# Kernel tuning notes

Measured on AMD Instinct MI355X. Metric: run time of the kernel, lower is better.

Reference implementation:

```python
import jax, jax.numpy as jnp
import numpy as np

B, C, H, W = 2, 128, 64, 64
EPS = 1e-5


def setup_inputs() -> dict:
    key = jax.random.key(0)
    ks = jax.random.split(key, 8)
    sc = 1.0 / np.sqrt(C)
    inp = {
        "x": jax.random.normal(ks[0], (B, C, H, W, 2), jnp.float32),
        # naive complex BN affine params: per-channel, per-component (real/imag)
        "bn_w": jnp.ones((C, 2), jnp.float32),
        "bn_b": jnp.zeros((C, 2), jnp.float32),
        # complex 1x1 conv weights: (out_c, in_c, 2) -> [..,0]=W_real, [..,1]=W_imag
        "wq": jax.random.normal(ks[1], (C, C, 2), jnp.float32) * sc,
        "bq": jnp.zeros((C, 2), jnp.float32),
        "wk": jax.random.normal(ks[2], (C, C, 2), jnp.float32) * sc,
        "bk": jnp.zeros((C, 2), jnp.float32),
        "wv": jax.random.normal(ks[3], (C, C, 2), jnp.float32) * sc,
        "bv": jnp.zeros((C, 2), jnp.float32),
        "gamma": jnp.float32(0.05),
    }
    return inp


def _complex_bn(x, w, b):
    # naive complex BN: normalize real and imag independently per channel
    # x: (B,C,H,W,2); stats over (B,H,W) per (C, component)
    mean = x.mean(axis=(0, 2, 3), keepdims=True)
    var = x.var(axis=(0, 2, 3), keepdims=True)
    xn = (x - mean) * jax.lax.rsqrt(var + EPS)
    return xn * w[None, :, None, None, :] + b[None, :, None, None, :]


def _complex_conv1x1(x, w, b):
    # x: (B,C,H,W,2); w: (O,C,2); b: (O,2)
    xr, xi = x[..., 0], x[..., 1]
    wr, wi = w[..., 0], w[..., 1]
    yr = jnp.einsum('oc,bchw->bohw', wr, xr) - jnp.einsum('oc,bchw->bohw', wi, xi)
    yi = jnp.einsum('oc,bchw->bohw', wr, xi) + jnp.einsum('oc,bchw->bohw', wi, xr)
    yr = yr + b[:, 0][None, :, None, None]
    yi = yi + b[:, 1][None, :, None, None]
    return jnp.stack([yr, yi], axis=-1)


def _attention(x, wq, bq, wk, bk, wv, bv, gamma):
    scale = C ** (-0.5)
    N = H * W
    # q,k,v: (B,C,H,W,2) -> (B,C,N,2) -> (B,N,C,2)
    to_tokens = lambda t: t.reshape(B, C, N, 2).transpose(0, 2, 1, 3)
    q = to_tokens(_complex_conv1x1(x, wq, bq))
    k = to_tokens(_complex_conv1x1(x, wk, bk))
    v = to_tokens(_complex_conv1x1(x, wv, bv))

    qr, qi = q[..., 0], q[..., 1]          # (B,N,C)
    kr, ki = k[..., 0], -k[..., 1]         # conjugate of k
    # k_t = conj(k) with token/channel axes swapped -> (B,C,N)
    ktr = kr.transpose(0, 2, 1)
    kti = ki.transpose(0, 2, 1)

    # complex matmul q @ k_t -> only the real part is used downstream
    attn_real = jnp.einsum('bnc,bcm->bnm', qr, ktr) - jnp.einsum('bnc,bcm->bnm', qi, kti)
    attn_w = jax.nn.softmax(attn_real * scale, axis=-1)  # (B,N,N)
    # dropout = identity (eval mode)

    # attn is purely real -> complex matmul reduces to two real matmuls
    out_r = jnp.einsum('bnm,bmc->bnc', attn_w, v[..., 0])
    out_i = jnp.einsum('bnm,bmc->bnc', attn_w, v[..., 1])
    out = jnp.stack([out_r, out_i], axis=-1)              # (B,N,C,2)
    out = out.transpose(0, 2, 1, 3).reshape(B, C, H, W, 2)
    return x + gamma * out


def reference(x, bn_w, bn_b, wq, bq, wk, bk, wv, bv, gamma):
    xn = _complex_bn(x, bn_w, bn_b)
    return _attention(xn, wq, bq, wk, bk, wv, bv, gamma)
```

## Files before the change

### kernel.cpp

```cpp
#include <hip/hip_runtime.h>
#include <hip/hip_bf16.h>
#include <hip/hip_fp8.h>

typedef __bf16 bf16_t;
typedef __bf16 bf16x8 __attribute__((ext_vector_type(8)));
typedef float  f32x4  __attribute__((ext_vector_type(4)));
typedef long   i64_t;

#define MFMA16(A,B,C) __builtin_amdgcn_mfma_f32_16x16x32_bf16((A),(B),(C),0,0,0)
#define MFMA8(A,B,C)  __builtin_amdgcn_mfma_f32_16x16x32_fp8_fp8((A),(B),(C),0,0,0)
#define MFMA85(A,B,C) __builtin_amdgcn_mfma_f32_16x16x32_bf8_fp8((A),(B),(C),0,0,0)

constexpr int Bn = 2, Cc = 128, Hh = 64, Wd = 64;
constexpr int N  = Hh * Wd;
constexpr int T  = Bn * N;
constexpr int D  = 2 * Cc;
constexpr int NSP = 4;
constexpr float EPS = 1e-5f;
constexpr float SCL = 0.08838834764831845f * 1.4426950408889634f;
constexpr float PSH = 9.0f;

__device__ __forceinline__ int tfrag(int row, int ch) {
    return (((ch >> 5) * 4 + (row >> 4)) << 10) +
           ((((ch >> 3) & 3) * 16 + (row & 15)) << 4) + (ch & 7) * 2;
}

__device__ __forceinline__ void gl16(const void* g, void* l) {
    __builtin_amdgcn_global_load_lds(
        (const __attribute__((address_space(1))) void*)g,
        (__attribute__((address_space(3))) void*)l, 16, 0, 0);
}

__global__ void k_pre(const float* __restrict__ x, float4* __restrict__ part,
                      const float* __restrict__ wq, const float* __restrict__ wk,
                      const float* __restrict__ wv, const float* __restrict__ bq,
                      const float* __restrict__ bk, const float* __restrict__ bv,
                      char* __restrict__ Wg, float* __restrict__ bt) {
    int tid = threadIdx.x;
    if (blockIdx.x < 512) {
        int bid = blockIdx.x;
        int q = bid >> 7, c = bid & 127;
        float sr = 0.f, si = 0.f, qr = 0.f, qi = 0.f;
        for (int b = 0; b < Bn; ++b) {
            const float4* p = (const float4*)((const float2*)x +
                              (size_t)(b * Cc + c) * N + q * 1024);
            for (int i = tid; i < 512; i += 256) {
                float4 v = p[i];
                sr += v.x + v.z; si += v.y + v.w;
                qr += v.x * v.x + v.z * v.z; qi += v.y * v.y + v.w * v.w;
            }
        }
        #pragma unroll
        for (int d = 32; d >= 1; d >>= 1) {
            sr += __shfl_xor(sr, d); si += __shfl_xor(si, d);
            qr += __shfl_xor(qr, d); qi += __shfl_xor(qi, d);
        }
        __shared__ float red[4][4];
        int w = tid >> 6;
        if ((tid & 63) == 0) { red[w][0] = sr; red[w][1] = si; red[w][2] = qr; red[w][3] = qi; }
        __syncthreads();
        if (tid == 0) {
            part[c * 4 + q] = make_float4(red[0][0] + red[1][0] + red[2][0] + red[3][0],
                                          red[0][1] + red[1][1] + red[2][1] + red[3][1],
                                          red[0][2] + red[1][2] + red[2][2] + red[3][2],
                                          red[0][3] + red[1][3] + red[2][3] + red[3][3]);
        }
    } else {
        int o = blockIdx.x - 512;
        int k = tid;
        int proj = o >> 8, oc = o & 255;
        const float* wsrc = proj == 0 ? wq : (proj == 1 ? wk : wv);
        const float* bsrc = proj == 0 ? bq : (proj == 1 ? bk : bv);
        int co = oc >> 7, oo = oc & 127;
        int c = k & 127, kc = k >> 7;
        float val;
        if (co == 0) val = (kc == 0) ? wsrc[(oo * 128 + c) * 2 + 0] : -wsrc[(oo * 128 + c) * 2 + 1];
        else         val = (kc == 0) ? wsrc[(oo * 128 + c) * 2 + 1] :  wsrc[(oo * 128 + c) * 2 + 0];
        int tile = o >> 6, row = o & 63;
        *(bf16_t*)(Wg + (size_t)tile * 32768 + tfrag(row, k)) = (bf16_t)val;
        if (k == 0) bt[o] = bsrc[oo * 2 + co];
    }
}

__global__ void k_norm(const float* __restrict__ x, const float4* __restrict__ part,
                       const float* __restrict__ bn_w, const float* __restrict__ bn_b,
                       char* __restrict__ XNg) {
    __shared__ float4 ssl[128];
    __shared__ __align__(16) char Tsh[32768];
    int blk = blockIdx.x;
    int b = blk >> 6, hw0 = (blk & 63) * 64;
    int tid = threadIdx.x;
    if (tid < 128) {
        float4 p0 = part[tid * 4 + 0], p1 = part[tid * 4 + 1];
        float4 p2 = part[tid * 4 + 2], p3 = part[tid * 4 + 3];
        float sr = p0.x + p1.x + p2.x + p3.x, si = p0.y + p1.y + p2.y + p3.y;
        float qr = p0.z + p1.z + p2.z + p3.z, qi = p0.w + p1.w + p2.w + p3.w;
        const float inv = 1.0f / (float)(Bn * N);
        float mr = sr * inv, mi = si * inv;
        float vr = qr * inv - mr * mr, vi = qi * inv - mi * mi;
        float scr = bn_w[tid * 2 + 0] * rsqrtf(vr + EPS);
        float sci = bn_w[tid * 2 + 1] * rsqrtf(vi + EPS);
        ssl[tid] = make_float4(scr, bn_b[tid * 2 + 0] - mr * scr,
                               sci, bn_b[tid * 2 + 1] - mi * sci);
    }
    __syncthreads();
    const float4* xin4 = (const float4*)x;
    #pragma unroll
    for (int it = 0; it < 16; ++it) {
        int idx = it * 256 + tid;
        int c = idx >> 5, h2 = (idx & 31) * 2;
        size_t gi = ((size_t)(b * Cc + c) * N + hw0 + h2) >> 1;
        float4 v = xin4[gi];
        float4 s = ssl[c];
        *(bf16_t*)(Tsh + tfrag(h2, c))           = (bf16_t)(v.x * s.x + s.y);
        *(bf16_t*)(Tsh + tfrag(h2, c + 128))     = (bf16_t)(v.y * s.z + s.w);
        *(bf16_t*)(Tsh + tfrag(h2 + 1, c))       = (bf16_t)(v.z * s.x + s.y);
        *(bf16_t*)(Tsh + tfrag(h2 + 1, c + 128)) = (bf16_t)(v.w * s.z + s.w);
    }
    __syncthreads();
    #pragma unroll
    for (int it = 0; it < 8; ++it) {
        int idx = it * 256 + tid;
        *(uint4*)(XNg + (size_t)blk * 32768 + idx * 16) = *(const uint4*)(Tsh + idx * 16);
    }
}

__global__ __launch_bounds__(256) void k_qkv(const char* __restrict__ XNg,
        const char* __restrict__ Wg, const float* __restrict__ bt,
        char* __restrict__ Qg, char* __restrict__ Kg, char* __restrict__ Vg) {
    __shared__ __align__(16) char Xsh[32768];
    __shared__ __align__(16) char Wsh[32768];
    int mx = blockIdx.x, ny = blockIdx.y;
    int tid = threadIdx.x;
    int w = tid >> 6, lane = tid & 63, n15 = lane & 15, quad = lane >> 4;
    const char* xs = XNg + (size_t)mx * 32768;
    const char* wsp = Wg + (size_t)ny * 32768;
    #pragma unroll
    for (int i = 0; i < 8; ++i) {
        int off = (w * 8 + i) * 1024 + lane * 16;
        gl16(xs + off, Xsh + off);
        gl16(wsp + off, Wsh + off);
    }
    __syncthreads();
    f32x4 acc[4] = {};
    #pragma unroll
    for (int ks = 0; ks < 8; ++ks) {
        bf16x8 a = *(const bf16x8*)(Xsh + (ks * 4 + w) * 1024 + lane * 16);
        #pragma unroll
        for (int t = 0; t < 4; ++t) {
            bf16x8 bw = *(const bf16x8*)(Wsh + (ks * 4 + t) * 1024 + lane * 16);
            acc[t] = MFMA16(a, bw, acc[t]);
        }
    }
    int proj = ny >> 2;
    int jb = (ny & 3) * 64;
    __syncthreads();
    char* Osh = Xsh;
    #pragma unroll
    for (int t = 0; t < 4; ++t) {
        float bias = bt[ny * 64 + t * 16 + n15];
        unsigned w01 = (unsigned)__builtin_amdgcn_cvt_pk_fp8_f32(
            acc[t][0] + bias, acc[t][1] + bias, 0, false);
        unsigned w23 = (unsigned)__builtin_amdgcn_cvt_pk_fp8_f32(
            acc[t][2] + bias, acc[t][3] + bias, 0, false);
        unsigned char vb[4] = {(unsigned char)(w01 & 0xff), (unsigned char)((w01 >> 8) & 0xff),
                               (unsigned char)(w23 & 0xff), (unsigned char)((w23 >> 8) & 0xff)};
        #pragma unroll
        for (int r = 0; r < 4; ++r) {
            if (proj < 2) {
                int lf  = (t >> 1) * 4 + w;
                int lif = (((2 * t + (n15 >> 3)) & 3) << 4) + quad * 4 + r;
                Osh[lf * 512 + lif * 8 + (n15 & 7)] = vb[r];
            } else {
                int key = w * 16 + quad * 4 + r;
                int lf  = (w >> 1) * 4 + t;
                int lif = (((key >> 3) & 3) << 4) + n15;
                Osh[lf * 512 + lif * 8 + (key & 7)] = vb[r];
            }
        }
    }
    __syncthreads();
    {
        int lf = tid >> 5, sub = (tid & 31) * 16;
        size_t tile = (size_t)mx;
        int gfrag = (proj < 2) ? ((jb >> 5) * 4 + lf)
                               : ((lf >> 2) * 16 + (jb >> 4) + (lf & 3));
        char* dst = (proj == 0 ? Qg : (proj == 1 ? Kg : Vg));
        *(uint4*)(dst + tile * 16384 + (size_t)gfrag * 512 + sub) =
            *(const uint4*)(Osh + tid * 16);
    }
}

__global__ __launch_bounds__(256) void k_attn(const char* __restrict__ Qg,
        const char* __restrict__ Kg, const char* __restrict__ Vg,
        bf16_t* __restrict__ Opb, float* __restrict__ Lp) {
    __shared__ __align__(16) char Ksh[2 * 16384];
    __shared__ __align__(16) char Vsh[2 * 16384];
    __shared__ __align__(16) char Psh[4096];
    int bid = blockIdx.x;
    int grp = bid & 7, qt = bid >> 3;
    int sp = grp & 3, b = grp >> 2;
    int tid = threadIdx.x;
    int w = tid >> 6, lane = tid & 63, n15 = lane & 15, quad = lane >> 4;
    int r = w >> 1, h = w & 1;

    const i64_t ONES = 0x3838383838383838L;

    i64_t qf[2][8];
    const char* qb = Qg + (size_t)(b * 64 + qt) * 16384;
    #pragma unroll
    for (int g = 0; g < 2; ++g)
        #pragma unroll
        for (int ks = 0; ks < 8; ++ks)
            qf[g][ks] = *(const i64_t*)(qb + ((ks * 4 + r * 2 + g) << 9) + lane * 8);

    f32x4 o[2][8] = {};
    f32x4 l_[2] = {};

    size_t kbase = (size_t)(b * 64 + sp * 16) * 16384;
    #pragma unroll
    for (int i = 0; i < 4; ++i) {
        int off = (w * 4 + i) * 1024 + lane * 16;
        gl16(Kg + kbase + off, Ksh + off);
        gl16(Vg + kbase + off, Vsh + off);
    }

    for (int kt = 0; kt < 16; ++kt) {
        int cur = kt & 1;
        asm volatile("s_waitcnt vmcnt(0)" ::: "memory");
        __builtin_amdgcn_s_barrier();
        __builtin_amdgcn_sched_barrier(0);

        if (kt < 15) {
            size_t tb = kbase + (size_t)(kt + 1) * 16384;
            char* kb = Ksh + (cur ^ 1) * 16384;
            char* vb = Vsh + (cur ^ 1) * 16384;
            #pragma unroll
            for (int i = 0; i < 4; ++i) {
                int off = (w * 4 + i) * 1024 + lane * 16;
                gl16(Kg + tb + off, kb + off);
                gl16(Vg + tb + off, vb + off);
            }
        }

        const char* kc = Ksh + cur * 16384;
        f32x4 s[2][2] = {};
        #pragma unroll
        for (int ks = 0; ks < 8; ++ks) {
            #pragma unroll
            for (int c = 0; c < 2; ++c) {
                i64_t kf = *(const i64_t*)(kc + ((ks * 4 + h * 2 + c) << 9) + lane * 8);
                s[0][c] = MFMA8(qf[0][ks], kf, s[0][c]);
                s[1][c] = MFMA8(qf[1][ks], kf, s[1][c]);
            }
        }
        #pragma unroll
        for (int g = 0; g < 2; ++g)
            #pragma unroll
            for (int c = 0; c < 2; ++c) {
                float p0 = __builtin_amdgcn_exp2f(s[g][c][0] * SCL - PSH);
                float p1 = __builtin_amdgcn_exp2f(s[g][c][1] * SCL - PSH);
                float p2 = __builtin_amdgcn_exp2f(s[g][c][2] * SCL - PSH);
                float p3 = __builtin_amdgcn_exp2f(s[g][c][3] * SCL - PSH);
                unsigned w01 = (unsigned)__builtin_amdgcn_cvt_pk_bf8_f32(p0, p1, 0, false);
                unsigned w23 = (unsigned)__builtin_amdgcn_cvt_pk_bf8_f32(p2, p3, 0, false);
                char* pb = Psh + ((h * 4 + r * 2 + g) << 9) +
                           (((c * 2 + (n15 >> 3)) * 16 + quad * 4) << 3) + (n15 & 7);
                pb[0]  = (unsigned char)(w01 & 0xff);
                pb[8]  = (unsigned char)((w01 >> 8) & 0xff);
                pb[16] = (unsigned char)(w23 & 0xff);
                pb[24] = (unsigned char)((w23 >> 8) & 0xff);
            }
        asm volatile("s_waitcnt lgkmcnt(0)" ::: "memory");
        __builtin_amdgcn_s_barrier();
        __builtin_amdgcn_sched_barrier(0);

        const char* vc = Vsh + cur * 16384;
        #pragma unroll
        for (int k2 = 0; k2 < 2; ++k2) {
            i64_t pa0 = *(const i64_t*)(Psh + ((k2 * 4 + r * 2 + 0) << 9) + lane * 8);
            i64_t pa1 = *(const i64_t*)(Psh + ((k2 * 4 + r * 2 + 1) << 9) + lane * 8);
            l_[0] = MFMA85(pa0, ONES, l_[0]);
            l_[1] = MFMA85(pa1, ONES, l_[1]);
            #pragma unroll
            for (int ct = 0; ct < 8; ++ct) {
                i64_t vf = *(const i64_t*)(vc + ((k2 * 16 + h * 8 + ct) << 9) + lane * 8);
                o[0][ct] = MFMA85(pa0, vf, o[0][ct]);
                o[1][ct] = MFMA85(pa1, vf, o[1][ct]);
            }
        }
    }
    int tok0 = b * N + qt * 64 + r * 32;
    #pragma unroll
    for (int g = 0; g < 2; ++g) {
        #pragma unroll
        for (int ct = 0; ct < 8; ++ct)
            #pragma unroll
            for (int ri = 0; ri < 4; ++ri)
                Opb[((size_t)sp * T + tok0 + g * 16 + quad * 4 + ri) * D +
                    h * 128 + ct * 16 + n15] = (bf16_t)o[g][ct][ri];
        if (h == 0 && n15 == 0) {
            #pragma unroll
            for (int ri = 0; ri < 4; ++ri)
                Lp[sp * T + tok0 + g * 16 + quad * 4 + ri] = l_[g][ri];
        }
    }
}

__global__ void k_comb(const bf16_t* __restrict__ Opb, const float* __restrict__ Lp,
                       const float4* __restrict__ part, const float* __restrict__ bn_w,
                       const float* __restrict__ bn_b, const float* __restrict__ x,
                       const float* __restrict__ gamma, float* __restrict__ out) {
    __shared__ float4 ssl[128];
    __shared__ float wts[16];
    __shared__ float Ot[256 * 17];
    int blk = blockIdx.x;
    int b = blk >> 8, hw0 = (blk & 255) * 16;
    int tok0 = b * N + hw0;
    int tid = threadIdx.x;
    if (tid < 128) {
        float4 p0 = part[tid * 4 + 0], p1 = part[tid * 4 + 1];
        float4 p2 = part[tid * 4 + 2], p3 = part[tid * 4 + 3];
        float sr = p0.x + p1.x + p2.x + p3.x, si = p0.y + p1.y + p2.y + p3.y;
        float qr = p0.z + p1.z + p2.z + p3.z, qi = p0.w + p1.w + p2.w + p3.w;
        const float inv = 1.0f / (float)(Bn * N);
        float mr = sr * inv, mi = si * inv;
        float vr = qr * inv - mr * mr, vi = qi * inv - mi * mi;
        float scr = bn_w[tid * 2 + 0] * rsqrtf(vr + EPS);
        float sci = bn_w[tid * 2 + 1] * rsqrtf(vi + EPS);
        ssl[tid] = make_float4(scr, bn_b[tid * 2 + 0] - mr * scr,
                               sci, bn_b[tid * 2 + 1] - mi * sci);
    }
    if (tid < 16) {
        float Z = 0.f;
        #pragma unroll
        for (int s = 0; s < NSP; ++s) Z += Lp[s * T + tok0 + tid];
        wts[tid] = gamma[0] / Z;
    }
    __syncthreads();
    #pragma unroll
    for (int i = 0; i < 2; ++i) {
        int idx = i * 256 + tid;
        int tk = idx >> 5, chunk = idx & 31;
        size_t base = (size_t)(tok0 + tk) * D + chunk * 8;
        float acc[8] = {};
        #pragma unroll
        for (int s = 0; s < NSP; ++s) {
            bf16x8 v = *(const bf16x8*)(Opb + (size_t)s * T * D + base);
            #pragma unroll
            for (int j = 0; j < 8; ++j) acc[j] += (float)v[j];
        }
        float ww = wts[tk];
        #pragma unroll
        for (int j = 0; j < 8; ++j) Ot[(chunk * 8 + j) * 17 + tk] = acc[j] * ww;
    }
    __syncthreads();
    const float2* xin = (const float2*)x;
    float2* xo = (float2*)out;
    #pragma unroll
    for (int i = 0; i < 8; ++i) {
        int linear = i * 256 + tid;
        int c = linear >> 4, hwo = linear & 15;
        size_t idx = (size_t)(b * Cc + c) * N + hw0 + hwo;
        float2 v = xin[idx];
        float4 s = ssl[c];
        float2 res;
        res.x = v.x * s.x + s.y + Ot[c * 17 + hwo];
        res.y = v.y * s.z + s.w + Ot[(128 + c) * 17 + hwo];
        xo[idx] = res;
    }
}

extern "C" void kernel_launch(void* const* d_in, const int* in_sizes, int n_in,
                              void* d_out, int out_size, void* d_ws, size_t ws_size,
                              hipStream_t stream) {
    const float* x    = (const float*)d_in[0];
    const float* bn_w = (const float*)d_in[1];
    const float* bn_b = (const float*)d_in[2];
    const float* wq   = (const float*)d_in[3];
    const float* bq   = (const float*)d_in[4];
    const float* wk   = (const float*)d_in[5];
    const float* bk   = (const float*)d_in[6];
    const float* wv   = (const float*)d_in[7];
    const float* bv   = (const float*)d_in[8];
    const float* gam  = (const float*)d_in[9];
    float* out = (float*)d_out;

    char* ws = (char*)d_ws;
    size_t off = 0;
    auto alloc = [&](size_t bytes) -> void* {
        void* p = ws + off;
        off += (bytes + 255) & ~(size_t)255;
        return p;
    };
    float4* part = (float4*)alloc(512 * sizeof(float4));
    char*   XNg  = (char*)alloc((size_t)128 * 32768);
    char*   Wg   = (char*)alloc((size_t)12 * 32768);
    float*  bt   = (float*)alloc(768 * 4);
    char*   Qg   = (char*)alloc((size_t)128 * 16384);
    char*   Kg   = (char*)alloc((size_t)128 * 16384);
    char*   Vg   = (char*)alloc((size_t)128 * 16384);
    bf16_t* Opb  = (bf16_t*)alloc((size_t)NSP * T * D * 2);
    float*  Lp   = (float*)alloc((size_t)NSP * T * 4);

    k_pre<<<1280, 256, 0, stream>>>(x, part, wq, wk, wv, bq, bk, bv, Wg, bt);
    k_norm<<<128, 256, 0, stream>>>(x, part, bn_w, bn_b, XNg);
    k_qkv<<<dim3(128, 12), 256, 0, stream>>>(XNg, Wg, bt, Qg, Kg, Vg);
    k_attn<<<512, 256, 0, stream>>>(Qg, Kg, Vg, Opb, Lp);
    k_comb<<<512, 256, 0, stream>>>(Opb, Lp, part, bn_w, bn_b, x, gam, out);
}
```

Baseline: 141.6 us.

## Fuse batch-norm into QKV projection kernel, drop XN staging buffer

Merges the normalization kernel into the QKV projection. Each block now normalizes its x tile directly into shared memory and loops over four weight tiles per projection, so the grid shrinks from 128x12 to 128x3. This removes one kernel launch and the global write and read of the normalized bf16 activations. In exchange, each x tile is normalized three times (once per projection), there are fewer blocks to fill the GPU, and the four weight tiles are processed serially without overlap.

```diff
diff --git a/kernel.cpp b/kernel.cpp
--- a/kernel.cpp
+++ b/kernel.cpp
@@ -82,14 +82,19 @@
     }
 }
 
-__global__ void k_norm(const float* __restrict__ x, const float4* __restrict__ part,
-                       const float* __restrict__ bn_w, const float* __restrict__ bn_b,
-                       char* __restrict__ XNg) {
+__global__ __launch_bounds__(256) void k_qkv(const float* __restrict__ x,
+        const float4* __restrict__ part, const float* __restrict__ bn_w,
+        const float* __restrict__ bn_b, const char* __restrict__ Wg,
+        const float* __restrict__ bt,
+        char* __restrict__ Qg, char* __restrict__ Kg, char* __restrict__ Vg) {
     __shared__ float4 ssl[128];
-    __shared__ __align__(16) char Tsh[32768];
-    int blk = blockIdx.x;
-    int b = blk >> 6, hw0 = (blk & 63) * 64;
+    __shared__ __align__(16) char Xsh[32768];
+    __shared__ __align__(16) char Wsh[32768];
+    __shared__ __align__(16) char Osh[4096];
+    int mx = blockIdx.x, proj = blockIdx.y;
     int tid = threadIdx.x;
+    int w = tid >> 6, lane = tid & 63, n15 = lane & 15, quad = lane >> 4;
+
     if (tid < 128) {
         float4 p0 = part[tid * 4 + 0], p1 = part[tid * 4 + 1];
         float4 p2 = part[tid * 4 + 2], p3 = part[tid * 4 + 3];
@@ -104,90 +109,78 @@
                                sci, bn_b[tid * 2 + 1] - mi * sci);
     }
     __syncthreads();
-    const float4* xin4 = (const float4*)x;
-    #pragma unroll
-    for (int it = 0; it < 16; ++it) {
-        int idx = it * 256 + tid;
-        int c = idx >> 5, h2 = (idx & 31) * 2;
-        size_t gi = ((size_t)(b * Cc + c) * N + hw0 + h2) >> 1;
-        float4 v = xin4[gi];
-        float4 s = ssl[c];
-        *(bf16_t*)(Tsh + tfrag(h2, c))           = (bf16_t)(v.x * s.x + s.y);
-        *(bf16_t*)(Tsh + tfrag(h2, c + 128))     = (bf16_t)(v.y * s.z + s.w);
-        *(bf16_t*)(Tsh + tfrag(h2 + 1, c))       = (bf16_t)(v.z * s.x + s.y);
-        *(bf16_t*)(Tsh + tfrag(h2 + 1, c + 128)) = (bf16_t)(v.w * s.z + s.w);
-    }
-    __syncthreads();
-    #pragma unroll
-    for (int it = 0; it < 8; ++it) {
-        int idx = it * 256 + tid;
-        *(uint4*)(XNg + (size_t)blk * 32768 + idx * 16) = *(const uint4*)(Tsh + idx * 16);
-    }
-}
-
-__global__ __launch_bounds__(256) void k_qkv(const char* __restrict__ XNg,
-        const char* __restrict__ Wg, const float* __restrict__ bt,
-        char* __restrict__ Qg, char* __restrict__ Kg, char* __restrict__ Vg) {
-    __shared__ __align__(16) char Xsh[32768];
-    __shared__ __align__(16) char Wsh[32768];
-    int mx = blockIdx.x, ny = blockIdx.y;
-    int tid = threadIdx.x;
-    int w = tid >> 6, lane = tid & 63, n15 = lane & 15, quad = lane >> 4;
-    const char* xs = XNg + (size_t)mx * 32768;
-    const char* wsp = Wg + (size_t)ny * 32768;
-    #pragma unroll
-    for (int i = 0; i < 8; ++i) {
-        int off = (w * 8 + i) * 1024 + lane * 16;
-        gl16(xs + off, Xsh + off);
-        gl16(wsp + off, Wsh + off);
-    }
-    __syncthreads();
-    f32x4 acc[4] = {};
-    #pragma unroll
-    for (int ks = 0; ks < 8; ++ks) {
-        bf16x8 a = *(const bf16x8*)(Xsh + (ks * 4 + w) * 1024 + lane * 16);
+    {
+        int b = mx >> 6, hw0 = (mx & 63) * 64;
+        const float4* xin4 = (const float4*)x;
+        #pragma unroll
+        for (int it = 0; it < 16; ++it) {
+            int idx = it * 256 + tid;
+            int c = idx >> 5, h2 = (idx & 31) * 2;
+            size_t gi = ((size_t)(b * Cc + c) * N + hw0 + h2) >> 1;
+            float4 v = xin4[gi];
+            float4 s = ssl[c];
+            *(bf16_t*)(Xsh + tfrag(h2, c))           = (bf16_t)(v.x * s.x + s.y);
+            *(bf16_t*)(Xsh + tfrag(h2, c + 128))     = (bf16_t)(v.y * s.z + s.w);
+            *(bf16_t*)(Xsh + tfrag(h2 + 1, c))       = (bf16_t)(v.z * s.x + s.y);
+            *(bf16_t*)(Xsh + tfrag(h2 + 1, c + 128)) = (bf16_t)(v.w * s.z + s.w);
+        }
+    }
+
+    for (int p = 0; p < 4; ++p) {
+        int ny = proj * 4 + p, jb = p * 64;
+        __syncthreads();
+        const char* wsp = Wg + (size_t)ny * 32768;
+        #pragma unroll
+        for (int i = 0; i < 8; ++i) {
+            int off = (w * 8 + i) * 1024 + lane * 16;
+            gl16(wsp + off, Wsh + off);
+        }
+        __syncthreads();
+
+        f32x4 acc[4] = {};
+        #pragma unroll
+        for (int ks = 0; ks < 8; ++ks) {
+            bf16x8 a = *(const bf16x8*)(Xsh + (ks * 4 + w) * 1024 + lane * 16);
+            #pragma unroll
+            for (int t = 0; t < 4; ++t) {
+                bf16x8 bw = *(const bf16x8*)(Wsh + (ks * 4 + t) * 1024 + lane * 16);
+                acc[t] = MFMA16(a, bw, acc[t]);
+            }
+        }
+        __syncthreads();
+
         #pragma unroll
         for (int t = 0; t < 4; ++t) {
-            bf16x8 bw = *(const bf16x8*)(Wsh + (ks * 4 + t) * 1024 + lane * 16);
-            acc[t] = MFMA16(a, bw, acc[t]);
-        }
-    }
-    int proj = ny >> 2;
-    int jb = (ny & 3) * 64;
-    __syncthreads();
-    char* Osh = Xsh;
-    #pragma unroll
-    for (int t = 0; t < 4; ++t) {
-        float bias = bt[ny * 64 + t * 16 + n15];
-        unsigned w01 = (unsigned)__builtin_amdgcn_cvt_pk_fp8_f32(
-            acc[t][0] + bias, acc[t][1] + bias, 0, false);
-        unsigned w23 = (unsigned)__builtin_amdgcn_cvt_pk_fp8_f32(
-            acc[t][2] + bias, acc[t][3] + bias, 0, false);
-        unsigned char vb[4] = {(unsigned char)(w01 & 0xff), (unsigned char)((w01 >> 8) & 0xff),
-                               (unsigned char)(w23 & 0xff), (unsigned char)((w23 >> 8) & 0xff)};
-        #pragma unroll
-        for (int r = 0; r < 4; ++r) {
-            if (proj < 2) {
-                int lf  = (t >> 1) * 4 + w;
-                int lif = (((2 * t + (n15 >> 3)) & 3) << 4) + quad * 4 + r;
-                Osh[lf * 512 + lif * 8 + (n15 & 7)] = vb[r];
-            } else {
-                int key = w * 16 + quad * 4 + r;
-                int lf  = (w >> 1) * 4 + t;
-                int lif = (((key >> 3) & 3) << 4) + n15;
-                Osh[lf * 512 + lif * 8 + (key & 7)] = vb[r];
-            }
-        }
-    }
-    __syncthreads();
-    {
-        int lf = tid >> 5, sub = (tid & 31) * 16;
-        size_t tile = (size_t)mx;
-        int gfrag = (proj < 2) ? ((jb >> 5) * 4 + lf)
-                               : ((lf >> 2) * 16 + (jb >> 4) + (lf & 3));
-        char* dst = (proj == 0 ? Qg : (proj == 1 ? Kg : Vg));
-        *(uint4*)(dst + tile * 16384 + (size_t)gfrag * 512 + sub) =
-            *(const uint4*)(Osh + tid * 16);
+            float bias = bt[ny * 64 + t * 16 + n15];
+            unsigned w01 = (unsigned)__builtin_amdgcn_cvt_pk_fp8_f32(
+                acc[t][0] + bias, acc[t][1] + bias, 0, false);
+            unsigned w23 = (unsigned)__builtin_amdgcn_cvt_pk_fp8_f32(
+                acc[t][2] + bias, acc[t][3] + bias, 0, false);
+            unsigned char vb[4] = {(unsigned char)(w01 & 0xff), (unsigned char)((w01 >> 8) & 0xff),
+                                   (unsigned char)(w23 & 0xff), (unsigned char)((w23 >> 8) & 0xff)};
+            #pragma unroll
+            for (int r = 0; r < 4; ++r) {
+                if (proj < 2) {
+                    int lf  = (t >> 1) * 4 + w;
+                    int lif = (((2 * t + (n15 >> 3)) & 3) << 4) + quad * 4 + r;
+                    Osh[lf * 512 + lif * 8 + (n15 & 7)] = vb[r];
+                } else {
+                    int key = w * 16 + quad * 4 + r;
+                    int lf  = (w >> 1) * 4 + t;
+                    int lif = (((key >> 3) & 3) << 4) + n15;
+                    Osh[lf * 512 + lif * 8 + (key & 7)] = vb[r];
+                }
+            }
+        }
+        __syncthreads();
+        {
+            int lf = tid >> 5, sub = (tid & 31) * 16;
+            int gfrag = (proj < 2) ? ((jb >> 5) * 4 + lf)
+                                   : ((lf >> 2) * 16 + (jb >> 4) + (lf & 3));
+            char* dst = (proj == 0 ? Qg : (proj == 1 ? Kg : Vg));
+            *(uint4*)(dst + (size_t)mx * 16384 + (size_t)gfrag * 512 + sub) =
+                *(const uint4*)(Osh + tid * 16);
+        }
     }
 }
 
@@ -394,7 +387,6 @@
         return p;
     };
     float4* part = (float4*)alloc(512 * sizeof(float4));
-    char*   XNg  = (char*)alloc((size_t)128 * 32768);
     char*   Wg   = (char*)alloc((size_t)12 * 32768);
     float*  bt   = (float*)alloc(768 * 4);
     char*   Qg   = (char*)alloc((size_t)128 * 16384);
@@ -404,8 +396,7 @@
     float*  Lp   = (float*)alloc((size_t)NSP * T * 4);
 
     k_pre<<<1280, 256, 0, stream>>>(x, part, wq, wk, wv, bq, bk, bv, Wg, bt);
-    k_norm<<<128, 256, 0, stream>>>(x, part, bn_w, bn_b, XNg);
-    k_qkv<<<dim3(128, 12), 256, 0, stream>>>(XNg, Wg, bt, Qg, Kg, Vg);
+    k_qkv<<<dim3(128, 3), 256, 0, stream>>>(x, part, bn_w, bn_b, Wg, bt, Qg, Kg, Vg);
     k_attn<<<512, 256, 0, stream>>>(Qg, Kg, Vg, Opb, Lp);
     k_comb<<<512, 256, 0, stream>>>(Opb, Lp, part, bn_w, bn_b, x, gam, out);
 }
```

New measurement: 142.2 us (median of 2 runs). About the same (+0.4%).
